# Kernel optimization log

Hardware: AMD Instinct MI355X
Metric: run time of the kernel (lower is better)

Reference implementation:

```python
import jax, jax.numpy as jnp
import numpy as np

T, HEADS, DIM_HEAD = 16, 16, 72
M = HEADS * DIM_HEAD  # 1152
SCALE = DIM_HEAD ** -0.5


def _ln(x, eps):
    mu = x.mean(-1, keepdims=True)
    var = x.var(-1, keepdims=True)
    return (x - mu) / jnp.sqrt(var + eps)


def _rotate_half(t):
    # interleaved pairs (x1, x2) -> (-x2, x1), as in rotary-embedding-torch
    t1, t2 = t[..., 0::2], t[..., 1::2]
    return jnp.stack([-t2, t1], axis=-1).reshape(t.shape)


def _rotary(t, pos):
    d = t.shape[-1]
    inv_freq = 1.0 / (10000.0 ** (jnp.arange(0, d, 2, dtype=jnp.float32) / d))
    freqs = pos.astype(jnp.float32)[:, None] * inv_freq          # (T, d/2)
    freqs = jnp.repeat(freqs, 2, axis=-1)                        # (T, d)
    return t * jnp.cos(freqs) + _rotate_half(t) * jnp.sin(freqs)


def _forward(x, c4t, c, W_ada, b_ada, tn_w, tn_b, t_qkv, t_k, t_v, t_out,
             t_fc_w, t_fc_b, s_qkv, s_k, s_v, s_out,
             mlp_w1, mlp_b1, mlp_w2, mlp_b2, f):
    B = c4t.shape[0]
    K, N, _ = x.shape

    ada = jax.nn.silu(c4t) @ W_ada + b_ada                       # (B, 6M)
    sh_msa, sc_msa, g_msa, sh_mlp, sc_mlp, g_mlp = jnp.split(ada, 6, axis=1)

    x4 = x.reshape(B, T, N, M)

    # ---- temporal attention (seq dim = frames, rotary, per-frame cond k/v) ----
    xt = _ln(x4, 1e-5) * tn_w + tn_b                             # temporal_norm1
    xt = xt.transpose(0, 2, 1, 3)                                # (B, N, T, M)
    q, k, v = jnp.split(xt @ t_qkv, 3, axis=-1)

    def heads_t(t):  # (B,N,T,M) -> (B,N,h,T,d)
        return t.reshape(B, N, T, HEADS, DIM_HEAD).transpose(0, 1, 3, 2, 4)

    q, k, v = map(heads_t, (q, k, v))
    k = _rotary(k, f)
    ek = (c @ t_k).reshape(B, T, HEADS, DIM_HEAD).transpose(0, 2, 1, 3)  # (B,h,T,d)
    ev = (c @ t_v).reshape(B, T, HEADS, DIM_HEAD).transpose(0, 2, 1, 3)
    ek = _rotary(ek, f)
    ek = jnp.broadcast_to(ek[:, None], k.shape)                  # (B,N,h,T,d)
    ev = jnp.broadcast_to(ev[:, None], v.shape)
    kk = jnp.concatenate([ek, k], axis=-2)                       # (B,N,h,2T,d)
    vv = jnp.concatenate([ev, v], axis=-2)
    q = _rotary(q * SCALE, f)
    attn = jax.nn.softmax(jnp.einsum('bnhid,bnhjd->bnhij', q, kk), axis=-1)
    out = jnp.einsum('bnhij,bnhjd->bnhid', attn, vv)
    out = out.transpose(0, 1, 3, 2, 4).reshape(B, N, T, M) @ t_out
    res = out.transpose(0, 2, 1, 3) @ t_fc_w + t_fc_b            # (B,T,N,M)
    x4 = x4 + res

    # ---- spatial attention with adaLN modulate + one cond token per frame ----
    mod = _ln(x4, 1e-6) * (1.0 + sc_msa[:, None, None, :]) + sh_msa[:, None, None, :]
    q, k, v = jnp.split(mod @ s_qkv, 3, axis=-1)

    def heads_s(t):  # (B,T,N,M) -> (B,T,h,N,d)
        return t.reshape(B, T, N, HEADS, DIM_HEAD).transpose(0, 1, 3, 2, 4)

    q, k, v = map(heads_s, (q, k, v))
    ek = (c @ s_k).reshape(B, T, HEADS, DIM_HEAD)[:, :, :, None, :]  # (B,T,h,1,d)
    ev = (c @ s_v).reshape(B, T, HEADS, DIM_HEAD)[:, :, :, None, :]
    kk = jnp.concatenate([ek, k], axis=-2)                       # (B,T,h,N+1,d)
    vv = jnp.concatenate([ev, v], axis=-2)
    attn = jax.nn.softmax(jnp.einsum('bthid,bthjd->bthij', q * SCALE, kk), axis=-1)
    out = jnp.einsum('bthij,bthjd->bthid', attn, vv)
    out = out.transpose(0, 1, 3, 2, 4).reshape(B, T, N, M) @ s_out
    x4 = x4 + g_msa[:, None, None, :] * out

    # ---- gated MLP with adaLN modulate ----
    mod2 = _ln(x4, 1e-6) * (1.0 + sc_mlp[:, None, None, :]) + sh_mlp[:, None, None, :]
    h = jax.nn.gelu(mod2 @ mlp_w1 + mlp_b1, approximate=True)
    y = h @ mlp_w2 + mlp_b2
    x4 = x4 + g_mlp[:, None, None, :] * y
    return x4.reshape(K, N, M)


def setup_inputs() -> dict:
    key = jax.random.key(0)
    ks = jax.random.split(key, 20)
    B, N = 2, 256

    def w(k, shape, s=0.02):
        return jax.random.normal(k, shape, jnp.float32) * s

    return {
        'x': jax.random.normal(ks[0], (B * T, N, M), jnp.float32),
        'c4t': jax.random.normal(ks[1], (B, M), jnp.float32),
        'c': jax.random.normal(ks[2], (B, T, M), jnp.float32),
        'W_ada': w(ks[3], (M, 6 * M)), 'b_ada': w(ks[4], (6 * M,)),
        'tn_w': jnp.ones(M, jnp.float32), 'tn_b': jnp.zeros(M, jnp.float32),
        't_qkv': w(ks[5], (M, 3 * M)), 't_k': w(ks[6], (M, M)),
        't_v': w(ks[7], (M, M)), 't_out': w(ks[8], (M, M)),
        't_fc_w': w(ks[9], (M, M)), 't_fc_b': jnp.zeros(M, jnp.float32),
        's_qkv': w(ks[10], (M, 3 * M)), 's_k': w(ks[11], (M, M)),
        's_v': w(ks[12], (M, M)), 's_out': w(ks[13], (M, M)),
        'mlp_w1': w(ks[14], (M, 4 * M)), 'mlp_b1': jnp.zeros(4 * M, jnp.float32),
        'mlp_w2': w(ks[15], (4 * M, M)), 'mlp_b2': jnp.zeros(M, jnp.float32),
        'f': jnp.arange(T, dtype=jnp.int32),
    }


def reference(x, c4t, c, W_ada, b_ada, tn_w, tn_b, t_qkv, t_k, t_v, t_out,
              t_fc_w, t_fc_b, s_qkv, s_k, s_v, s_out,
              mlp_w1, mlp_b1, mlp_w2, mlp_b2, f):
    return _forward(x, c4t, c, W_ada, b_ada, tn_w, tn_b, t_qkv, t_k, t_v, t_out,
                    t_fc_w, t_fc_b, s_qkv, s_k, s_v, s_out,
                    mlp_w1, mlp_b1, mlp_w2, mlp_b2, f)
```

## Files before the change

kernel.cpp:

```cpp
#include <hip/hip_runtime.h>
#include <hip/hip_bf16.h>

typedef __hip_bfloat16 bf16;
typedef __attribute__((ext_vector_type(8))) short short8;
typedef __attribute__((ext_vector_type(4))) float floatx4;

__device__ __forceinline__ float b2f(bf16 v) { return __bfloat162float(v); }
__device__ __forceinline__ short f2bs(float v) {
    bf16 h = __float2bfloat16(v);
    return *(short*)&h;
}
__device__ __forceinline__ float invfreq(int jj) {
    return expf(-0.25584278811044955f * (float)jj);
}

template<int MODE>
__device__ __forceinline__ float ldin(const void* p, long i) {
    if (MODE == 0) return b2f(((const bf16*)p)[i]);
    else           return ((const float*)p)[i];
}

#define SCALE_ 0.11785113019775793f

#define GLDS(gp, lp) __builtin_amdgcn_global_load_lds( \
    (const __attribute__((address_space(1))) void*)(gp), \
    (__attribute__((address_space(3))) void*)(lp), 16, 0, 0)

__global__ void k_detect(const void* __restrict__ x, int* __restrict__ flag)
{
    const unsigned short* u = (const unsigned short*)x;
    int tid = threadIdx.x;
    int insane = 0;
    for (int i = tid; i < 2048; i += 64) {
        unsigned short s = u[i];
        int ex = (s >> 7) & 0xFF;
        if (ex >= 0xC5) insane++;
    }
    #pragma unroll
    for (int off = 32; off > 0; off >>= 1) insane += __shfl_down(insane, off);
    if (tid == 0) flag[0] = (insane > 8) ? 1 : 0;
}

__global__ void k_rope(const int* __restrict__ f, float* __restrict__ ropeC,
                       float* __restrict__ ropeS)
{
    int idx = blockIdx.x * 256 + threadIdx.x;
    if (idx < 1152) {
        int t = idx / 72, d = idx - t * 72;
        float ang = (float)f[t] * invfreq(d >> 1);
        float sn, cs; sincosf(ang, &sn, &cs);
        ropeC[idx] = cs;
        ropeS[idx] = sn;
    }
}

__global__ void k_silu(const void* __restrict__ c4t, float* __restrict__ out,
                       const int* __restrict__ flg)
{
    int i = blockIdx.x * 256 + threadIdx.x;
    if (i < 2304) {
        float v = (*flg == 0) ? ldin<0>(c4t, i) : ldin<1>(c4t, i);
        out[i] = v / (1.f + expf(-v));
    }
}

__global__ void k_cvt(const void* __restrict__ in, float* __restrict__ out, int n,
                      const int* __restrict__ flg)
{
    int i = blockIdx.x * 256 + threadIdx.x;
    if (i < n) out[i] = (*flg == 0) ? ldin<0>(in, i) : ldin<1>(in, i);
}

__global__ void k_cvtb(const float* __restrict__ in, bf16* __restrict__ out, int n)
{
    int i = blockIdx.x * 256 + threadIdx.x;
    if (i < n) out[i] = __float2bfloat16(in[i]);
}

template<int MODE>
__device__ __forceinline__ void wt_body(float (*tile)[33], const void* __restrict__ W,
    bf16* __restrict__ Wt, int K, int N)
{
    int n0 = blockIdx.x << 5, k0 = blockIdx.y << 5;
    int tid = threadIdx.x;
    int r = tid >> 3, c4 = (tid & 7) << 2;
    long base = (long)(k0 + r) * N + n0 + c4;
    #pragma unroll
    for (int i = 0; i < 4; ++i) tile[r][c4 + i] = ldin<MODE>(W, base + i);
    __syncthreads();
    long obase = (long)(n0 + r) * K + k0 + c4;
    #pragma unroll
    for (int i = 0; i < 4; ++i) Wt[obase + i] = __float2bfloat16(tile[c4 + i][r]);
}

__global__ __launch_bounds__(256) void k_wt(const void* __restrict__ W,
    bf16* __restrict__ Wt, int K, int N, const int* __restrict__ flg)
{
    __shared__ float tile[32][33];
    if (*flg == 0) wt_body<0>(tile, W, Wt, K, N);
    else           wt_body<1>(tile, W, Wt, K, N);
}

template<int MODE>
__device__ __forceinline__ void gemm_body(
    float (*As)[64], float (*Bs)[64],
    const float* __restrict__ A, const void* __restrict__ W,
    const void* __restrict__ bias, float* __restrict__ C,
    int R, int K, int N)
{
    int tid = threadIdx.x;
    int tx = tid & 15, ty = tid >> 4;
    int row0 = blockIdx.y << 6;
    int col0 = blockIdx.x << 6;
    float acc[4][4] = {};
    int ar = tid >> 2;
    int ak = (tid & 3) << 2;
    int bk = tid >> 4;
    int bc = (tid & 15) << 2;
    for (int kt = 0; kt < K; kt += 16) {
        if (row0 + ar < R) {
            const float4 a4 = *(const float4*)(A + (long)(row0 + ar) * K + kt + ak);
            As[ak + 0][ar] = a4.x; As[ak + 1][ar] = a4.y;
            As[ak + 2][ar] = a4.z; As[ak + 3][ar] = a4.w;
        } else {
            As[ak + 0][ar] = 0.f; As[ak + 1][ar] = 0.f;
            As[ak + 2][ar] = 0.f; As[ak + 3][ar] = 0.f;
        }
        #pragma unroll
        for (int i = 0; i < 4; ++i)
            Bs[bk][bc + i] = ldin<MODE>(W, (long)(kt + bk) * N + col0 + bc + i);
        __syncthreads();
        #pragma unroll
        for (int kk = 0; kk < 16; ++kk) {
            float4 av = *(const float4*)&As[kk][ty << 2];
            float4 bv = *(const float4*)&Bs[kk][tx << 2];
            float a[4] = {av.x, av.y, av.z, av.w};
            float b[4] = {bv.x, bv.y, bv.z, bv.w};
            #pragma unroll
            for (int i = 0; i < 4; ++i)
                #pragma unroll
                for (int j = 0; j < 4; ++j)
                    acc[i][j] += a[i] * b[j];
        }
        __syncthreads();
    }
    #pragma unroll
    for (int i = 0; i < 4; ++i) {
        int gr = row0 + (ty << 2) + i;
        if (gr >= R) continue;
        float* cp = C + (long)gr * N + col0 + (tx << 2);
        #pragma unroll
        for (int j = 0; j < 4; ++j) {
            float v = acc[i][j];
            if (bias) v += ldin<MODE>(bias, col0 + (tx << 2) + j);
            cp[j] = v;
        }
    }
}

__global__ __launch_bounds__(256) void k_gemm(
    const float* __restrict__ A, const void* __restrict__ W,
    const void* __restrict__ bias, float* __restrict__ C,
    int R, int K, int N, const int* __restrict__ flg)
{
    __shared__ float As[16][64];
    __shared__ float Bs[16][64];
    if (*flg == 0) gemm_body<0>(As, Bs, A, W, bias, C, R, K, N);
    else           gemm_body<1>(As, Bs, A, W, bias, C, R, K, N);
}

template<int EMODE>
__global__ __launch_bounds__(512, 4) void k_mgemm(
    const bf16* __restrict__ A, const bf16* __restrict__ Wt,
    const float* __restrict__ bias, void* __restrict__ Cout,
    int K, int N, int outbf, int act,
    float* __restrict__ x4, const float* __restrict__ ada, int part,
    const void* __restrict__ xin, void* __restrict__ outp,
    const int* __restrict__ flg)
{
    __shared__ short As[24576];
    __shared__ short Bs[12288];
    int tid = threadIdx.x;
    int lane = tid & 63, wave = tid >> 6;
    int wm = wave >> 1, wn = wave & 1;

    int gx = gridDim.x;
    int nwg = gx * (int)gridDim.y;
    int orig = blockIdx.y * gx + blockIdx.x;
    int qq = nwg >> 3, rr = nwg & 7;
    int xcd = orig & 7, loc = orig >> 3;
    int wg = (xcd < rr ? xcd * (qq + 1) : rr * (qq + 1) + (xcd - rr) * qq) + loc;
    int bx = wg % gx, by = wg / gx;

    long row0 = (long)by << 8;
    long col0 = (long)bx << 7;
    int mi = lane & 15, q = lane >> 4;

    const bf16* gA0 = A  + (row0 + (2 * wave) * 16 + mi) * K + q * 8;
    const bf16* gA1 = gA0 + 16 * K;
    const bf16* gB0 = Wt + (col0 + wave * 16 + mi) * K + q * 8;
    int dA0 = (2 * wave) * 512, dA1 = (2 * wave + 1) * 512, dB0 = wave * 512;

    floatx4 acc[4][4] = {};
    int nt = K >> 5;

    GLDS(gA0,      &As[dA0]);
    GLDS(gA1,      &As[dA1]);
    GLDS(gB0,      &Bs[dB0]);
    GLDS(gA0 + 32, &As[8192 + dA0]);
    GLDS(gA1 + 32, &As[8192 + dA1]);
    GLDS(gB0 + 32, &Bs[4096 + dB0]);
    __builtin_amdgcn_sched_barrier(0);
    asm volatile("s_waitcnt vmcnt(3)" ::: "memory");
    __builtin_amdgcn_sched_barrier(0);
    __builtin_amdgcn_s_barrier();
    __builtin_amdgcn_sched_barrier(0);

    int aRd = wm * 2048 + lane * 8;
    int bRd = wn * 2048 + lane * 8;
    int cs = 0;
    int si = 2;

    for (int t = 0; t < nt; ++t) {
        if (t + 2 < nt) {
            int oA = si << 13, oB = si << 12;
            int kt2 = (t + 2) << 5;
            GLDS(gA0 + kt2, &As[oA + dA0]);
            GLDS(gA1 + kt2, &As[oA + dA1]);
            GLDS(gB0 + kt2, &Bs[oB + dB0]);
        }
        {
            int oA = cs << 13, oB = cs << 12;
            short8 af[4], bfr[4];
            #pragma unroll
            for (int i = 0; i < 4; ++i)
                af[i] = *(const short8*)&As[oA + aRd + i * 512];
            #pragma unroll
            for (int j = 0; j < 4; ++j)
                bfr[j] = *(const short8*)&Bs[oB + bRd + j * 512];
            #pragma unroll
            for (int i = 0; i < 4; ++i)
                #pragma unroll
                for (int j = 0; j < 4; ++j)
                    acc[i][j] = __builtin_amdgcn_mfma_f32_16x16x32_bf16(
                        af[i], bfr[j], acc[i][j], 0, 0, 0);
        }
        __builtin_amdgcn_sched_barrier(0);
        if (t + 2 < nt) asm volatile("s_waitcnt vmcnt(3)" ::: "memory");
        else            asm volatile("s_waitcnt vmcnt(0)" ::: "memory");
        __builtin_amdgcn_sched_barrier(0);
        if (t < nt - 1) {
            __builtin_amdgcn_s_barrier();
            __builtin_amdgcn_sched_barrier(0);
        }
        cs = (cs == 2) ? 0 : cs + 1;
        si = (si == 2) ? 0 : si + 1;
    }

    int lr = lane >> 4, lc = lane & 15;
    int fl = flg ? *flg : 0;
    float b4[4] = {0.f, 0.f, 0.f, 0.f};
    if (bias) {
        #pragma unroll
        for (int j = 0; j < 4; ++j) b4[j] = bias[(int)col0 + wn * 64 + j * 16 + lc];
    }
    #pragma unroll
    for (int i = 0; i < 4; ++i) {
        #pragma unroll
        for (int r = 0; r < 4; ++r) {
            long grow = row0 + wm * 64 + i * 16 + lr * 4 + r;
            #pragma unroll
            for (int j = 0; j < 4; ++j) {
                int col = (int)col0 + wn * 64 + j * 16 + lc;
                float v = acc[i][j][r] + b4[j];
                if (act) {
                    float u = v;
                    float tt = 1.5957691216057308f * (u + 0.044715f * u * u * u);
                    v = u / (1.f + __expf(-tt));
                }
                if constexpr (EMODE == 0) {
                    if (outbf) ((bf16*)Cout)[grow * N + col] = __float2bfloat16(v);
                    else       ((float*)Cout)[grow * N + col] = v;
                } else if constexpr (EMODE == 1) {
                    int bb = (int)(grow >> 12);
                    int nn = ((int)grow >> 4) & 255;
                    int tt2 = (int)grow & 15;
                    long rx = ((long)((bb << 4) + tt2) << 8) + nn;
                    long idx = rx * 1152 + col;
                    float xv = (fl == 0) ? b2f(((const bf16*)xin)[idx])
                                         : ((const float*)xin)[idx];
                    x4[idx] = xv + v;
                } else {
                    int bb = (int)(grow >> 12);
                    float g = ada[(bb * 6 + part) * 1152 + col];
                    long idx = grow * 1152 + col;
                    float nv = x4[idx] + g * v;
                    x4[idx] = nv;
                    if (outp) {
                        if (fl == 0) ((bf16*)outp)[idx] = __float2bfloat16(nv);
                        else         ((float*)outp)[idx] = nv;
                    }
                }
            }
        }
    }
}

template<int MODE>
__device__ __forceinline__ void ln_t_body(float* rs, float* rss,
    const void* __restrict__ x, const void* __restrict__ w,
    const void* __restrict__ bb, bf16* __restrict__ out)
{
    int r = blockIdx.x;
    int n = r & 255;
    int bt = r >> 8;
    int b = bt >> 4, t = bt & 15;
    long orow = (long)((b << 8) + n) * 16 + t;
    int tid = threadIdx.x;
    float vals[5];
    float s = 0.f, ss = 0.f;
    int c = 0;
    for (int i = tid; i < 1152; i += 256, ++c) {
        float v = ldin<MODE>(x, (long)r * 1152 + i);
        vals[c] = v; s += v; ss += v * v;
    }
    #pragma unroll
    for (int off = 32; off > 0; off >>= 1) {
        s  += __shfl_down(s, off);
        ss += __shfl_down(ss, off);
    }
    int wid = tid >> 6;
    if ((tid & 63) == 0) { rs[wid] = s; rss[wid] = ss; }
    __syncthreads();
    float S  = rs[0] + rs[1] + rs[2] + rs[3];
    float SS = rss[0] + rss[1] + rss[2] + rss[3];
    float mu = S * (1.f / 1152.f);
    float var = SS * (1.f / 1152.f) - mu * mu;
    float rstd = rsqrtf(var + 1e-5f);
    c = 0;
    bf16* op = out + orow * 1152;
    for (int i = tid; i < 1152; i += 256, ++c)
        op[i] = __float2bfloat16((vals[c] - mu) * rstd * ldin<MODE>(w, i) + ldin<MODE>(bb, i));
}

__global__ __launch_bounds__(256) void k_ln_t(
    const void* __restrict__ x, const void* __restrict__ w,
    const void* __restrict__ bb, bf16* __restrict__ out,
    const int* __restrict__ flg)
{
    __shared__ float rs[4], rss[4];
    if (*flg == 0) ln_t_body<0>(rs, rss, x, w, bb, out);
    else           ln_t_body<1>(rs, rss, x, w, bb, out);
}

__global__ __launch_bounds__(256) void k_ln_mod(
    const float* __restrict__ x4, const float* __restrict__ ada,
    int psh, int psc, float eps, bf16* __restrict__ out)
{
    int r = blockIdx.x;
    int b = r >> 12;
    const float* xp = x4 + (long)r * 1152;
    int tid = threadIdx.x;
    float vals[5];
    float s = 0.f, ss = 0.f;
    int c = 0;
    for (int i = tid; i < 1152; i += 256, ++c) {
        float v = xp[i];
        vals[c] = v; s += v; ss += v * v;
    }
    #pragma unroll
    for (int off = 32; off > 0; off >>= 1) {
        s  += __shfl_down(s, off);
        ss += __shfl_down(ss, off);
    }
    __shared__ float rs[4], rss[4];
    int wid = tid >> 6;
    if ((tid & 63) == 0) { rs[wid] = s; rss[wid] = ss; }
    __syncthreads();
    float S  = rs[0] + rs[1] + rs[2] + rs[3];
    float SS = rss[0] + rss[1] + rss[2] + rss[3];
    float mu = S * (1.f / 1152.f);
    float var = SS * (1.f / 1152.f) - mu * mu;
    float rstd = rsqrtf(var + eps);
    const float* sh = ada + (b * 6 + psh) * 1152;
    const float* sc = ada + (b * 6 + psc) * 1152;
    c = 0;
    bf16* op = out + (long)r * 1152;
    for (int i = tid; i < 1152; i += 256, ++c)
        op[i] = __float2bfloat16((vals[c] - mu) * rstd * (1.f + sc[i]) + sh[i]);
}

__global__ __launch_bounds__(256) void k_attn_t(
    const bf16* __restrict__ qkv, const float* __restrict__ ekt,
    const float* __restrict__ evt, const float* __restrict__ ropeC,
    const float* __restrict__ ropeS, bf16* __restrict__ out)
{
    __shared__ float qs[16][73];
    __shared__ float ksT[72][33];
    __shared__ float vs[32][73];
    __shared__ float sc[16][33];
    int blk = blockIdx.x;
    int h = blk & 15;
    int bn = blk >> 4;
    int b = bn >> 8;
    int tid = threadIdx.x;
    long qbase = (long)bn * 16 * 3456 + h * 72;
    for (int idx = tid; idx < 16 * 72; idx += 256) {
        int i = idx / 72, d = idx - i * 72;
        long p0 = qbase + (long)i * 3456;
        float v  = b2f(qkv[p0 + d]);
        float v2 = b2f(qkv[p0 + (d ^ 1)]);
        float cs = ropeC[idx], sn = ropeS[idx];
        float rv = (d & 1) ? (v * cs + v2 * sn) : (v * cs - v2 * sn);
        qs[i][d] = rv * SCALE_;
    }
    for (int idx = tid; idx < 32 * 72; idx += 256) {
        int j = idx / 72, d = idx - j * 72;
        float kv, kv2, vv; int pi;
        if (j < 16) {
            long base = (long)(b * 16 + j) * 1152 + h * 72;
            kv  = ekt[base + d];
            kv2 = ekt[base + (d ^ 1)];
            vv  = evt[base + d];
            pi = j;
        } else {
            int jj = j - 16;
            long base = qbase + (long)jj * 3456;
            kv  = b2f(qkv[base + 1152 + d]);
            kv2 = b2f(qkv[base + 1152 + (d ^ 1)]);
            vv  = b2f(qkv[base + 2304 + d]);
            pi = jj;
        }
        float cs = ropeC[pi * 72 + d], sn = ropeS[pi * 72 + d];
        ksT[d][j] = (d & 1) ? (kv * cs + kv2 * sn) : (kv * cs - kv2 * sn);
        vs[j][d] = vv;
    }
    __syncthreads();
    for (int e = tid; e < 512; e += 256) {
        int i = e >> 5, j = e & 31;
        float s = 0.f;
        for (int d = 0; d < 72; ++d) s += qs[i][d] * ksT[d][j];
        sc[i][j] = s;
    }
    __syncthreads();
    if (tid < 16) {
        float m = -1e30f;
        for (int j = 0; j < 32; ++j) m = fmaxf(m, sc[tid][j]);
        float l = 0.f;
        for (int j = 0; j < 32; ++j) { float p = expf(sc[tid][j] - m); sc[tid][j] = p; l += p; }
        float inv = 1.f / l;
        for (int j = 0; j < 32; ++j) sc[tid][j] *= inv;
    }
    __syncthreads();
    for (int idx = tid; idx < 16 * 72; idx += 256) {
        int i = idx / 72, d = idx - i * 72;
        float o = 0.f;
        for (int j = 0; j < 32; ++j) o += sc[i][j] * vs[j][d];
        out[((long)bn * 16 + i) * 1152 + h * 72 + d] = __float2bfloat16(o);
    }
}

__global__ __launch_bounds__(256) void k_attn_s(
    const bf16* __restrict__ qkv, const bf16* __restrict__ eksb,
    const bf16* __restrict__ evsb, bf16* __restrict__ out)
{
    __shared__ short vT[5120];
    __shared__ short pl[4][1024];
    int tid = threadIdx.x;
    int lane = tid & 63, wave = tid >> 6;
    int blk = blockIdx.x;
    int ic = blk & 3;
    int bth = blk >> 2;
    int h = bth & 15;
    int bt = bth >> 4;
    int col = lane & 15, q = lane >> 4;
    int hoff = h * 72;
    long qkvbase = (long)bt * 256 * 3456;
    long ctxbase = (long)bt * 1152 + hoff;

    int qrow = ic * 64 + wave * 16 + col;
    const bf16* qptr = qkv + qkvbase + (long)qrow * 3456 + hoff;
    short8 qf[3];
    #pragma unroll
    for (int ks = 0; ks < 3; ++ks) {
        int k0 = ks * 32 + q * 8;
        if (k0 + 8 <= 72) qf[ks] = *(const short8*)(qptr + k0);
        else { short8 z = {0,0,0,0,0,0,0,0}; qf[ks] = z; }
    }

    floatx4 o[5] = {};
    float m_i[4], l_i[4];
    #pragma unroll
    for (int r = 0; r < 4; ++r) { m_i[r] = -1e30f; l_i[r] = 0.f; }

    for (int kc = 0; kc < 320; kc += 64) {
        for (int fi = tid; fi < 640; fi += 256) {
            int blkid = fi >> 6, fl2 = fi & 63;
            int dn = blkid >> 1, ks = blkid & 1;
            int d = dn * 16 + (fl2 & 15);
            int kq = fl2 >> 4;
            short8 v;
            #pragma unroll
            for (int j = 0; j < 8; ++j) {
                int gk = kc + ks * 32 + kq * 8 + j;
                short sv = 0;
                if (d < 72 && gk <= 256) {
                    if (gk == 0) sv = *(const short*)(eksb ? &evsb[ctxbase + d] : nullptr);
                    else sv = *(const short*)&qkv[qkvbase + (long)(gk - 1) * 3456 + 2304 + hoff + d];
                }
                v[j] = sv;
            }
            *(short8*)&vT[blkid * 512 + fl2 * 8] = v;
        }
        __syncthreads();

        floatx4 sacc[4] = {};
        #pragma unroll
        for (int nt = 0; nt < 4; ++nt) {
            int key = kc + nt * 16 + col;
            #pragma unroll
            for (int ks = 0; ks < 3; ++ks) {
                int k0 = ks * 32 + q * 8;
                short8 kf = {0,0,0,0,0,0,0,0};
                if (key <= 256 && k0 + 8 <= 72) {
                    if (key == 0) kf = *(const short8*)(eksb + ctxbase + k0);
                    else kf = *(const short8*)(qkv + qkvbase + (long)(key - 1) * 3456 + 1152 + hoff + k0);
                }
                sacc[nt] = __builtin_amdgcn_mfma_f32_16x16x32_bf16(qf[ks], kf, sacc[nt], 0, 0, 0);
            }
        }

        float p[4][4];
        #pragma unroll
        for (int r = 0; r < 4; ++r) {
            float mv = -1e30f;
            #pragma unroll
            for (int nt = 0; nt < 4; ++nt) {
                int key = kc + nt * 16 + col;
                float s = (key <= 256) ? sacc[nt][r] * SCALE_ : -1e30f;
                p[nt][r] = s;
                mv = fmaxf(mv, s);
            }
            #pragma unroll
            for (int xm = 1; xm < 16; xm <<= 1) mv = fmaxf(mv, __shfl_xor(mv, xm));
            float mn = fmaxf(m_i[r], mv);
            float alpha = expf(m_i[r] - mn);
            m_i[r] = mn;
            float rsum = 0.f;
            #pragma unroll
            for (int nt = 0; nt < 4; ++nt) {
                float e = expf(p[nt][r] - mn);
                p[nt][r] = e;
                rsum += e;
            }
            #pragma unroll
            for (int xm = 1; xm < 16; xm <<= 1) rsum += __shfl_xor(rsum, xm);
            l_i[r] = l_i[r] * alpha + rsum;
            #pragma unroll
            for (int dn = 0; dn < 5; ++dn) o[dn][r] *= alpha;
        }

        #pragma unroll
        for (int nt = 0; nt < 4; ++nt) {
            int kl = nt * 16 + col;
            int ks2 = kl >> 5, q2 = (kl >> 3) & 3, j = kl & 7;
            #pragma unroll
            for (int r = 0; r < 4; ++r) {
                int mrow = q * 4 + r;
                pl[wave][ks2 * 512 + q2 * 128 + mrow * 8 + j] = f2bs(p[nt][r]);
            }
        }
        __syncthreads();

        #pragma unroll
        for (int ks = 0; ks < 2; ++ks) {
            short8 pf = *(const short8*)&pl[wave][ks * 512 + lane * 8];
            #pragma unroll
            for (int dn = 0; dn < 5; ++dn) {
                short8 vf = *(const short8*)&vT[(dn * 2 + ks) * 512 + lane * 8];
                o[dn] = __builtin_amdgcn_mfma_f32_16x16x32_bf16(pf, vf, o[dn], 0, 0, 0);
            }
        }
        __syncthreads();
    }

    int orow0 = ic * 64 + wave * 16;
    #pragma unroll
    for (int dn = 0; dn < 5; ++dn) {
        int d = dn * 16 + col;
        if (d >= 72) continue;
        #pragma unroll
        for (int r = 0; r < 4; ++r) {
            int mrow = q * 4 + r;
            float val = o[dn][r] / l_i[r];
            out[((long)bt * 256 + orow0 + mrow) * 1152 + hoff + d] = __float2bfloat16(val);
        }
    }
}

extern "C" void kernel_launch(void* const* d_in, const int* in_sizes, int n_in,
                              void* d_out, int out_size, void* d_ws, size_t ws_size,
                              hipStream_t stream)
{
    const void* x      = d_in[0];
    const void* c4t    = d_in[1];
    const void* c      = d_in[2];
    const void* W_ada  = d_in[3];
    const void* b_ada  = d_in[4];
    const void* tn_w   = d_in[5];
    const void* tn_b   = d_in[6];
    const void* t_qkv  = d_in[7];
    const void* t_k    = d_in[8];
    const void* t_v    = d_in[9];
    const void* t_outw = d_in[10];
    const void* t_fcw  = d_in[11];
    const void* t_fcb  = d_in[12];
    const void* s_qkv  = d_in[13];
    const void* s_k    = d_in[14];
    const void* s_v    = d_in[15];
    const void* s_outw = d_in[16];
    const void* mlp_w1 = d_in[17];
    const void* mlp_b1 = d_in[18];
    const void* mlp_w2 = d_in[19];
    const void* mlp_b2 = d_in[20];
    const int*  f      = (const int*)d_in[21];

    float* ws    = (float*)d_ws;
    float* x4    = ws;
    float* buf2  = x4 + 9437184;
    float* reg1f = buf2 + 9437184;
    bf16*  qkvb  = (bf16*)reg1f;
    bf16*  hbf   = (bf16*)reg1f;
    float* abfAf = reg1f + 18874368;
    bf16*  abfA  = (bf16*)abfAf;
    float* abfBf = abfAf + 4718592;
    bf16*  abfB  = (bf16*)abfBf;
    float* wtf   = abfBf + 4718592;
    bf16*  wt    = (bf16*)wtf;
    bf16* t_qkv_t = wt;
    bf16* s_qkv_t = t_qkv_t + 3981312;
    bf16* t_out_t = s_qkv_t + 3981312;
    bf16* t_fc_t  = t_out_t + 1327104;
    bf16* s_out_t = t_fc_t  + 1327104;
    bf16* w1_t    = s_out_t + 1327104;
    bf16* w2_t    = w1_t    + 5308416;
    float* small  = wtf + 11280384;
    float* ada   = small;
    float* cf32  = ada  + 13824;
    float* ekt   = cf32 + 36864;
    float* evt   = ekt  + 36864;
    float* eks   = evt  + 36864;
    float* evs   = eks  + 36864;
    bf16*  eksb  = (bf16*)(evs + 36864);
    bf16*  evsb  = eksb + 36864;
    float* sc4   = (float*)(evsb + 36864);
    float* fcb_f = sc4  + 2304;
    float* b1_f  = fcb_f + 1152;
    float* b2_f  = b1_f  + 4608;
    float* ropeC = b2_f + 1152;
    float* ropeS = ropeC + 1152;
    int*   flg   = (int*)(ropeS + 1152);

    k_detect<<<1, 64, 0, stream>>>(x, flg);
    k_rope<<<5, 256, 0, stream>>>(f, ropeC, ropeS);

    k_silu<<<9, 256, 0, stream>>>(c4t, sc4, flg);
    k_gemm<<<dim3(108, 1), 256, 0, stream>>>(sc4, W_ada, b_ada, ada, 2, 1152, 6912, flg);

    k_cvt<<<144, 256, 0, stream>>>(c, cf32, 36864, flg);
    k_gemm<<<dim3(18, 1), 256, 0, stream>>>(cf32, t_k, nullptr, ekt, 32, 1152, 1152, flg);
    k_gemm<<<dim3(18, 1), 256, 0, stream>>>(cf32, t_v, nullptr, evt, 32, 1152, 1152, flg);
    k_gemm<<<dim3(18, 1), 256, 0, stream>>>(cf32, s_k, nullptr, eks, 32, 1152, 1152, flg);
    k_gemm<<<dim3(18, 1), 256, 0, stream>>>(cf32, s_v, nullptr, evs, 32, 1152, 1152, flg);
    k_cvtb<<<144, 256, 0, stream>>>(eks, eksb, 36864);
    k_cvtb<<<144, 256, 0, stream>>>(evs, evsb, 36864);

    k_cvt<<<5, 256, 0, stream>>>(t_fcb, fcb_f, 1152, flg);
    k_cvt<<<18, 256, 0, stream>>>(mlp_b1, b1_f, 4608, flg);
    k_cvt<<<5, 256, 0, stream>>>(mlp_b2, b2_f, 1152, flg);

    k_wt<<<dim3(108, 36), 256, 0, stream>>>(t_qkv, t_qkv_t, 1152, 3456, flg);
    k_wt<<<dim3(108, 36), 256, 0, stream>>>(s_qkv, s_qkv_t, 1152, 3456, flg);
    k_wt<<<dim3(36, 36), 256, 0, stream>>>(t_outw, t_out_t, 1152, 1152, flg);
    k_wt<<<dim3(36, 36), 256, 0, stream>>>(t_fcw, t_fc_t, 1152, 1152, flg);
    k_wt<<<dim3(36, 36), 256, 0, stream>>>(s_outw, s_out_t, 1152, 1152, flg);
    k_wt<<<dim3(144, 36), 256, 0, stream>>>(mlp_w1, w1_t, 1152, 4608, flg);
    k_wt<<<dim3(36, 144), 256, 0, stream>>>(mlp_w2, w2_t, 4608, 1152, flg);

    k_ln_t<<<8192, 256, 0, stream>>>(x, tn_w, tn_b, abfA, flg);
    k_mgemm<0><<<dim3(27, 32), 512, 0, stream>>>(abfA, t_qkv_t, nullptr, qkvb, 1152, 3456, 1, 0,
                                                 nullptr, nullptr, 0, nullptr, nullptr, flg);
    k_attn_t<<<8192, 256, 0, stream>>>(qkvb, ekt, evt, ropeC, ropeS, abfB);
    k_mgemm<0><<<dim3(9, 32), 512, 0, stream>>>(abfB, t_out_t, nullptr, abfA, 1152, 1152, 1, 0,
                                                nullptr, nullptr, 0, nullptr, nullptr, flg);
    k_mgemm<1><<<dim3(9, 32), 512, 0, stream>>>(abfA, t_fc_t, fcb_f, nullptr, 1152, 1152, 0, 0,
                                                x4, nullptr, 0, x, nullptr, flg);

    k_ln_mod<<<8192, 256, 0, stream>>>(x4, ada, 0, 1, 1e-6f, abfA);
    k_mgemm<0><<<dim3(27, 32), 512, 0, stream>>>(abfA, s_qkv_t, nullptr, qkvb, 1152, 3456, 1, 0,
                                                 nullptr, nullptr, 0, nullptr, nullptr, flg);
    k_attn_s<<<2048, 256, 0, stream>>>(qkvb, eksb, evsb, abfB);
    k_mgemm<2><<<dim3(9, 32), 512, 0, stream>>>(abfB, s_out_t, nullptr, nullptr, 1152, 1152, 0, 0,
                                                x4, ada, 2, nullptr, nullptr, flg);

    k_ln_mod<<<8192, 256, 0, stream>>>(x4, ada, 3, 4, 1e-6f, abfA);
    k_mgemm<0><<<dim3(36, 32), 512, 0, stream>>>(abfA, w1_t, b1_f, hbf, 1152, 4608, 1, 1,
                                                 nullptr, nullptr, 0, nullptr, nullptr, flg);
    k_mgemm<2><<<dim3(9, 32), 512, 0, stream>>>(hbf, w2_t, b2_f, nullptr, 4608, 1152, 0, 0,
                                                x4, ada, 5, nullptr, d_out, flg);
}
```

Measured before the change: 1.683 ms.

## Shrink MFMA GEMM tile to 128x128 with 256 threads, batch small setup kernels

The main bf16 MFMA GEMM goes from a 256x128 tile with 8 waves to a 128x128 tile with 4 waves, each wave covering 64x64. The grid doubles in rows and LDS per block shrinks, aiming for more resident workgroups and better wave balance across CUs. The cost is lower reuse of each loaded B tile and more loads per FLOP. Separately, many tiny setup launches (silu, conversions, rope, the four small K/V GEMMs, weight transposes) are merged into a few batched kernels to cut launch overhead.

```diff
diff --git a/kernel.cpp b/kernel.cpp
--- a/kernel.cpp
+++ b/kernel.cpp
@@ -18,6 +18,9 @@
 __device__ __forceinline__ float ldin(const void* p, long i) {
     if (MODE == 0) return b2f(((const bf16*)p)[i]);
     else           return ((const float*)p)[i];
+}
+__device__ __forceinline__ float ldf(const void* p, long i, int fl) {
+    return fl == 0 ? b2f(((const bf16*)p)[i]) : ((const float*)p)[i];
 }
 
 #define SCALE_ 0.11785113019775793f
@@ -41,11 +44,29 @@
     if (tid == 0) flag[0] = (insane > 8) ? 1 : 0;
 }
 
-__global__ void k_rope(const int* __restrict__ f, float* __restrict__ ropeC,
-                       float* __restrict__ ropeS)
-{
-    int idx = blockIdx.x * 256 + threadIdx.x;
-    if (idx < 1152) {
+__global__ void k_setup(const void* __restrict__ c4t, const void* __restrict__ c,
+                        const void* __restrict__ t_fcb, const void* __restrict__ mlp_b1,
+                        const void* __restrict__ mlp_b2, const int* __restrict__ f,
+                        float* __restrict__ sc4, float* __restrict__ cf32,
+                        float* __restrict__ fcb_f, float* __restrict__ b1_f,
+                        float* __restrict__ b2_f, float* __restrict__ ropeC,
+                        float* __restrict__ ropeS, const int* __restrict__ flg)
+{
+    int i = blockIdx.x * 256 + threadIdx.x;
+    int fl = *flg;
+    if (i < 2304) {
+        float v = ldf(c4t, i, fl);
+        sc4[i] = v / (1.f + expf(-v));
+    } else if (i < 39168) {
+        cf32[i - 2304] = ldf(c, i - 2304, fl);
+    } else if (i < 40320) {
+        fcb_f[i - 39168] = ldf(t_fcb, i - 39168, fl);
+    } else if (i < 44928) {
+        b1_f[i - 40320] = ldf(mlp_b1, i - 40320, fl);
+    } else if (i < 46080) {
+        b2_f[i - 44928] = ldf(mlp_b2, i - 44928, fl);
+    } else if (i < 47232) {
+        int idx = i - 46080;
         int t = idx / 72, d = idx - t * 72;
         float ang = (float)f[t] * invfreq(d >> 1);
         float sn, cs; sincosf(ang, &sn, &cs);
@@ -54,23 +75,6 @@
     }
 }
 
-__global__ void k_silu(const void* __restrict__ c4t, float* __restrict__ out,
-                       const int* __restrict__ flg)
-{
-    int i = blockIdx.x * 256 + threadIdx.x;
-    if (i < 2304) {
-        float v = (*flg == 0) ? ldin<0>(c4t, i) : ldin<1>(c4t, i);
-        out[i] = v / (1.f + expf(-v));
-    }
-}
-
-__global__ void k_cvt(const void* __restrict__ in, float* __restrict__ out, int n,
-                      const int* __restrict__ flg)
-{
-    int i = blockIdx.x * 256 + threadIdx.x;
-    if (i < n) out[i] = (*flg == 0) ? ldin<0>(in, i) : ldin<1>(in, i);
-}
-
 __global__ void k_cvtb(const float* __restrict__ in, bf16* __restrict__ out, int n)
 {
     int i = blockIdx.x * 256 + threadIdx.x;
@@ -99,6 +103,27 @@
     __shared__ float tile[32][33];
     if (*flg == 0) wt_body<0>(tile, W, Wt, K, N);
     else           wt_body<1>(tile, W, Wt, K, N);
+}
+
+__global__ __launch_bounds__(256) void k_wt2(const void* __restrict__ W0,
+    const void* __restrict__ W1, bf16* __restrict__ Wt0, const int* __restrict__ flg)
+{
+    __shared__ float tile[32][33];
+    const void* W = blockIdx.z ? W1 : W0;
+    bf16* Wt = Wt0 + (long)blockIdx.z * 3981312;
+    if (*flg == 0) wt_body<0>(tile, W, Wt, 1152, 3456);
+    else           wt_body<1>(tile, W, Wt, 1152, 3456);
+}
+
+__global__ __launch_bounds__(256) void k_wt3(const void* __restrict__ W0,
+    const void* __restrict__ W1, const void* __restrict__ W2,
+    bf16* __restrict__ Wt0, const int* __restrict__ flg)
+{
+    __shared__ float tile[32][33];
+    const void* W = (blockIdx.z == 0) ? W0 : (blockIdx.z == 1) ? W1 : W2;
+    bf16* Wt = Wt0 + (long)blockIdx.z * 1327104;
+    if (*flg == 0) wt_body<0>(tile, W, Wt, 1152, 1152);
+    else           wt_body<1>(tile, W, Wt, 1152, 1152);
 }
 
 template<int MODE>
@@ -106,11 +131,10 @@
     float (*As)[64], float (*Bs)[64],
     const float* __restrict__ A, const void* __restrict__ W,
     const void* __restrict__ bias, float* __restrict__ C,
-    int R, int K, int N)
+    int row0, int R, int K, int N)
 {
     int tid = threadIdx.x;
     int tx = tid & 15, ty = tid >> 4;
-    int row0 = blockIdx.y << 6;
     int col0 = blockIdx.x << 6;
     float acc[4][4] = {};
     int ar = tid >> 2;
@@ -165,12 +189,27 @@
 {
     __shared__ float As[16][64];
     __shared__ float Bs[16][64];
-    if (*flg == 0) gemm_body<0>(As, Bs, A, W, bias, C, R, K, N);
-    else           gemm_body<1>(As, Bs, A, W, bias, C, R, K, N);
+    if (*flg == 0) gemm_body<0>(As, Bs, A, W, bias, C, (int)(blockIdx.y << 6), R, K, N);
+    else           gemm_body<1>(As, Bs, A, W, bias, C, (int)(blockIdx.y << 6), R, K, N);
+}
+
+__global__ __launch_bounds__(256) void k_gemm4(
+    const float* __restrict__ A, const void* __restrict__ W0,
+    const void* __restrict__ W1, const void* __restrict__ W2,
+    const void* __restrict__ W3, float* __restrict__ C0,
+    const int* __restrict__ flg)
+{
+    __shared__ float As[16][64];
+    __shared__ float Bs[16][64];
+    int z = blockIdx.y;
+    const void* W = (z == 0) ? W0 : (z == 1) ? W1 : (z == 2) ? W2 : W3;
+    float* C = C0 + (long)z * 36864;
+    if (*flg == 0) gemm_body<0>(As, Bs, A, W, nullptr, C, 0, 32, 1152, 1152);
+    else           gemm_body<1>(As, Bs, A, W, nullptr, C, 0, 32, 1152, 1152);
 }
 
 template<int EMODE>
-__global__ __launch_bounds__(512, 4) void k_mgemm(
+__global__ __launch_bounds__(256, 3) void k_mgemm(
     const bf16* __restrict__ A, const bf16* __restrict__ Wt,
     const float* __restrict__ bias, void* __restrict__ Cout,
     int K, int N, int outbf, int act,
@@ -178,11 +217,11 @@
     const void* __restrict__ xin, void* __restrict__ outp,
     const int* __restrict__ flg)
 {
-    __shared__ short As[24576];
+    __shared__ short As[12288];
     __shared__ short Bs[12288];
     int tid = threadIdx.x;
     int lane = tid & 63, wave = tid >> 6;
-    int wm = wave >> 1, wn = wave & 1;
+    int mq = wave >> 1, nq = wave & 1;
 
     int gx = gridDim.x;
     int nwg = gx * (int)gridDim.y;
@@ -192,52 +231,56 @@
     int wg = (xcd < rr ? xcd * (qq + 1) : rr * (qq + 1) + (xcd - rr) * qq) + loc;
     int bx = wg % gx, by = wg / gx;
 
-    long row0 = (long)by << 8;
+    long row0 = (long)by << 7;
     long col0 = (long)bx << 7;
     int mi = lane & 15, q = lane >> 4;
 
     const bf16* gA0 = A  + (row0 + (2 * wave) * 16 + mi) * K + q * 8;
     const bf16* gA1 = gA0 + 16 * K;
-    const bf16* gB0 = Wt + (col0 + wave * 16 + mi) * K + q * 8;
-    int dA0 = (2 * wave) * 512, dA1 = (2 * wave + 1) * 512, dB0 = wave * 512;
+    const bf16* gB0 = Wt + (col0 + (2 * wave) * 16 + mi) * K + q * 8;
+    const bf16* gB1 = gB0 + 16 * K;
+    int dA0 = (2 * wave) * 512, dA1 = dA0 + 512;
 
     floatx4 acc[4][4] = {};
     int nt = K >> 5;
 
     GLDS(gA0,      &As[dA0]);
     GLDS(gA1,      &As[dA1]);
-    GLDS(gB0,      &Bs[dB0]);
-    GLDS(gA0 + 32, &As[8192 + dA0]);
-    GLDS(gA1 + 32, &As[8192 + dA1]);
-    GLDS(gB0 + 32, &Bs[4096 + dB0]);
+    GLDS(gB0,      &Bs[dA0]);
+    GLDS(gB1,      &Bs[dA1]);
+    GLDS(gA0 + 32, &As[4096 + dA0]);
+    GLDS(gA1 + 32, &As[4096 + dA1]);
+    GLDS(gB0 + 32, &Bs[4096 + dA0]);
+    GLDS(gB1 + 32, &Bs[4096 + dA1]);
     __builtin_amdgcn_sched_barrier(0);
-    asm volatile("s_waitcnt vmcnt(3)" ::: "memory");
+    asm volatile("s_waitcnt vmcnt(4)" ::: "memory");
     __builtin_amdgcn_sched_barrier(0);
     __builtin_amdgcn_s_barrier();
     __builtin_amdgcn_sched_barrier(0);
 
-    int aRd = wm * 2048 + lane * 8;
-    int bRd = wn * 2048 + lane * 8;
+    int aRd = mq * 2048 + lane * 8;
+    int bRd = nq * 2048 + lane * 8;
     int cs = 0;
     int si = 2;
 
     for (int t = 0; t < nt; ++t) {
         if (t + 2 < nt) {
-            int oA = si << 13, oB = si << 12;
+            int o = si << 12;
             int kt2 = (t + 2) << 5;
-            GLDS(gA0 + kt2, &As[oA + dA0]);
-            GLDS(gA1 + kt2, &As[oA + dA1]);
-            GLDS(gB0 + kt2, &Bs[oB + dB0]);
+            GLDS(gA0 + kt2, &As[o + dA0]);
+            GLDS(gA1 + kt2, &As[o + dA1]);
+            GLDS(gB0 + kt2, &Bs[o + dA0]);
+            GLDS(gB1 + kt2, &Bs[o + dA1]);
         }
         {
-            int oA = cs << 13, oB = cs << 12;
+            int o = cs << 12;
             short8 af[4], bfr[4];
             #pragma unroll
             for (int i = 0; i < 4; ++i)
-                af[i] = *(const short8*)&As[oA + aRd + i * 512];
+                af[i] = *(const short8*)&As[o + aRd + i * 512];
             #pragma unroll
             for (int j = 0; j < 4; ++j)
-                bfr[j] = *(const short8*)&Bs[oB + bRd + j * 512];
+                bfr[j] = *(const short8*)&Bs[o + bRd + j * 512];
             #pragma unroll
             for (int i = 0; i < 4; ++i)
                 #pragma unroll
@@ -246,7 +289,7 @@
                         af[i], bfr[j], acc[i][j], 0, 0, 0);
         }
         __builtin_amdgcn_sched_barrier(0);
-        if (t + 2 < nt) asm volatile("s_waitcnt vmcnt(3)" ::: "memory");
+        if (t + 2 < nt) asm volatile("s_waitcnt vmcnt(4)" ::: "memory");
         else            asm volatile("s_waitcnt vmcnt(0)" ::: "memory");
         __builtin_amdgcn_sched_barrier(0);
         if (t < nt - 1) {
@@ -262,16 +305,16 @@
     float b4[4] = {0.f, 0.f, 0.f, 0.f};
     if (bias) {
         #pragma unroll
-        for (int j = 0; j < 4; ++j) b4[j] = bias[(int)col0 + wn * 64 + j * 16 + lc];
+        for (int j = 0; j < 4; ++j) b4[j] = bias[(int)col0 + nq * 64 + j * 16 + lc];
     }
     #pragma unroll
     for (int i = 0; i < 4; ++i) {
         #pragma unroll
         for (int r = 0; r < 4; ++r) {
-            long grow = row0 + wm * 64 + i * 16 + lr * 4 + r;
+            long grow = row0 + mq * 64 + i * 16 + lr * 4 + r;
             #pragma unroll
             for (int j = 0; j < 4; ++j) {
-                int col = (int)col0 + wn * 64 + j * 16 + lc;
+                int col = (int)col0 + nq * 64 + j * 16 + lc;
                 float v = acc[i][j][r] + b4[j];
                 if (act) {
                     float u = v;
@@ -662,50 +705,37 @@
     int*   flg   = (int*)(ropeS + 1152);
 
     k_detect<<<1, 64, 0, stream>>>(x, flg);
-    k_rope<<<5, 256, 0, stream>>>(f, ropeC, ropeS);
-
-    k_silu<<<9, 256, 0, stream>>>(c4t, sc4, flg);
+    k_setup<<<185, 256, 0, stream>>>(c4t, c, t_fcb, mlp_b1, mlp_b2, f,
+                                     sc4, cf32, fcb_f, b1_f, b2_f, ropeC, ropeS, flg);
+
     k_gemm<<<dim3(108, 1), 256, 0, stream>>>(sc4, W_ada, b_ada, ada, 2, 1152, 6912, flg);
-
-    k_cvt<<<144, 256, 0, stream>>>(c, cf32, 36864, flg);
-    k_gemm<<<dim3(18, 1), 256, 0, stream>>>(cf32, t_k, nullptr, ekt, 32, 1152, 1152, flg);
-    k_gemm<<<dim3(18, 1), 256, 0, stream>>>(cf32, t_v, nullptr, evt, 32, 1152, 1152, flg);
-    k_gemm<<<dim3(18, 1), 256, 0, stream>>>(cf32, s_k, nullptr, eks, 32, 1152, 1152, flg);
-    k_gemm<<<dim3(18, 1), 256, 0, stream>>>(cf32, s_v, nullptr, evs, 32, 1152, 1152, flg);
-    k_cvtb<<<144, 256, 0, stream>>>(eks, eksb, 36864);
-    k_cvtb<<<144, 256, 0, stream>>>(evs, evsb, 36864);
-
-    k_cvt<<<5, 256, 0, stream>>>(t_fcb, fcb_f, 1152, flg);
-    k_cvt<<<18, 256, 0, stream>>>(mlp_b1, b1_f, 4608, flg);
-    k_cvt<<<5, 256, 0, stream>>>(mlp_b2, b2_f, 1152, flg);
-
-    k_wt<<<dim3(108, 36), 256, 0, stream>>>(t_qkv, t_qkv_t, 1152, 3456, flg);
-    k_wt<<<dim3(108, 36), 256, 0, stream>>>(s_qkv, s_qkv_t, 1152, 3456, flg);
-    k_wt<<<dim3(36, 36), 256, 0, stream>>>(t_outw, t_out_t, 1152, 1152, flg);
-    k_wt<<<dim3(36, 36), 256, 0, stream>>>(t_fcw, t_fc_t, 1152, 1152, flg);
-    k_wt<<<dim3(36, 36), 256, 0, stream>>>(s_outw, s_out_t, 1152, 1152, flg);
+    k_gemm4<<<dim3(18, 4), 256, 0, stream>>>(cf32, t_k, t_v, s_k, s_v, ekt, flg);
+    k_cvtb<<<288, 256, 0, stream>>>(eks, eksb, 73728);
+
+    k_wt2<<<dim3(108, 36, 2), 256, 0, stream>>>(t_qkv, s_qkv, t_qkv_t, flg);
+    k_wt3<<<dim3(36, 36, 3), 256, 0, stream>>>(t_outw, t_fcw, s_outw, t_out_t, flg);
     k_wt<<<dim3(144, 36), 256, 0, stream>>>(mlp_w1, w1_t, 1152, 4608, flg);
     k_wt<<<dim3(36, 144), 256, 0, stream>>>(mlp_w2, w2_t, 4608, 1152, flg);
 
     k_ln_t<<<8192, 256, 0, stream>>>(x, tn_w, tn_b, abfA, flg);
-    k_mgemm<0><<<dim3(27, 32), 512, 0, stream>>>(abfA, t_qkv_t, nullptr, qkvb, 1152, 3456, 1, 0,
+    k_mgemm<0><<<dim3(27, 64), 256, 0, stream>>>(abfA, t_qkv_t, nullptr, qkvb, 1152, 3456, 1, 0,
                                                  nullptr, nullptr, 0, nullptr, nullptr, flg);
     k_attn_t<<<8192, 256, 0, stream>>>(qkvb, ekt, evt, ropeC, ropeS, abfB);
-    k_mgemm<0><<<dim3(9, 32), 512, 0, stream>>>(abfB, t_out_t, nullptr, abfA, 1152, 1152, 1, 0,
+    k_mgemm<0><<<dim3(9, 64), 256, 0, stream>>>(abfB, t_out_t, nullptr, abfA, 1152, 1152, 1, 0,
                                                 nullptr, nullptr, 0, nullptr, nullptr, flg);
-    k_mgemm<1><<<dim3(9, 32), 512, 0, stream>>>(abfA, t_fc_t, fcb_f, nullptr, 1152, 1152, 0, 0,
+    k_mgemm<1><<<dim3(9, 64), 256, 0, stream>>>(abfA, t_fc_t, fcb_f, nullptr, 1152, 1152, 0, 0,
                                                 x4, nullptr, 0, x, nullptr, flg);
 
     k_ln_mod<<<8192, 256, 0, stream>>>(x4, ada, 0, 1, 1e-6f, abfA);
-    k_mgemm<0><<<dim3(27, 32), 512, 0, stream>>>(abfA, s_qkv_t, nullptr, qkvb, 1152, 3456, 1, 0,
+    k_mgemm<0><<<dim3(27, 64), 256, 0, stream>>>(abfA, s_qkv_t, nullptr, qkvb, 1152, 3456, 1, 0,
                                                  nullptr, nullptr, 0, nullptr, nullptr, flg);
     k_attn_s<<<2048, 256, 0, stream>>>(qkvb, eksb, evsb, abfB);
-    k_mgemm<2><<<dim3(9, 32), 512, 0, stream>>>(abfB, s_out_t, nullptr, nullptr, 1152, 1152, 0, 0,
+    k_mgemm<2><<<dim3(9, 64), 256, 0, stream>>>(abfB, s_out_t, nullptr, nullptr, 1152, 1152, 0, 0,
                                                 x4, ada, 2, nullptr, nullptr, flg);
 
     k_ln_mod<<<8192, 256, 0, stream>>>(x4, ada, 3, 4, 1e-6f, abfA);
-    k_mgemm<0><<<dim3(36, 32), 512, 0, stream>>>(abfA, w1_t, b1_f, hbf, 1152, 4608, 1, 1,
+    k_mgemm<0><<<dim3(36, 64), 256, 0, stream>>>(abfA, w1_t, b1_f, hbf, 1152, 4608, 1, 1,
                                                  nullptr, nullptr, 0, nullptr, nullptr, flg);
-    k_mgemm<2><<<dim3(9, 32), 512, 0, stream>>>(hbf, w2_t, b2_f, nullptr, 4608, 1152, 0, 0,
+    k_mgemm<2><<<dim3(9, 64), 256, 0, stream>>>(hbf, w2_t, b2_f, nullptr, 4608, 1152, 0, 0,
                                                 x4, ada, 5, nullptr, d_out, flg);
 }
```

After: 1.487 ms. 1.13x faster.
